# Kernel optimization log

Hardware: AMD Instinct MI355X
Metric: run time of the kernel (lower is better)

Reference implementation:

```python
import jax, jax.numpy as jnp
import numpy as np
import math

B, T, D, H = 1, 2048, 1024, 16
DH = D // H  # 64


def relative_shift(x):
    # x: [B, H, T, S] -> Transformer-XL relative shift via zero-pad + reshape
    b, h, t, s = x.shape
    zero_pad = jnp.zeros((b, h, t, 1), dtype=x.dtype)
    x_padded = jnp.concatenate([zero_pad, x], axis=-1)       # [B,H,T,S+1]
    x_padded = x_padded.reshape(b, h, s + 1, t)              # [B,H,S+1,T]
    return x_padded[:, :, 1:].reshape(b, h, t, s)            # [B,H,T,S]


def setup_inputs() -> dict:
    key = jax.random.key(0)
    ks = jax.random.split(key, 9)
    std = 0.02
    return {
        "x": jax.random.normal(ks[0], (B, T, D), dtype=jnp.float32),
        "r_emb": jax.random.normal(ks[1], (T, D), dtype=jnp.float32),
        "Wq": jax.random.normal(ks[2], (D, D), dtype=jnp.float32) * std,
        "Wk": jax.random.normal(ks[3], (D, D), dtype=jnp.float32) * std,
        "Wv": jax.random.normal(ks[4], (D, D), dtype=jnp.float32) * std,
        "Wr": jax.random.normal(ks[5], (D, D), dtype=jnp.float32) * std,
        "Wo": jax.random.normal(ks[6], (D, D), dtype=jnp.float32) * std,
        "u": jax.random.normal(ks[7], (H, DH), dtype=jnp.float32) * std,
        "v_bias": jax.random.normal(ks[8], (H, DH), dtype=jnp.float32) * std,
    }


def reference(x, r_emb, Wq, Wk, Wv, Wr, Wo, u, v_bias):
    # mem=None path (the only shape-consistent path in the source), so S == T.
    b, t, d = x.shape
    s = t
    q = (x @ Wq).reshape(b, t, H, DH).transpose(0, 2, 1, 3)   # [B,H,T,DH]
    k = (x @ Wk).reshape(b, s, H, DH).transpose(0, 2, 1, 3)   # [B,H,S,DH]
    v = (x @ Wv).reshape(b, s, H, DH).transpose(0, 2, 1, 3)   # [B,H,S,DH]
    r = (r_emb @ Wr).reshape(r_emb.shape[0], H, DH)[-s:]       # [S,H,DH]

    AC = jnp.einsum('bhid,bhjd->bhij', q + u[None, :, None, :], k)
    BD = jnp.einsum('bhid,jhd->bhij', q + v_bias[None, :, None, :], r)
    BD = relative_shift(BD)

    attn = (AC + BD) / math.sqrt(DH)                           # [B,H,T,S]
    mask = jnp.tril(jnp.ones((t, s), dtype=bool))              # causal (S==T)
    attn = jnp.where(mask[None, None], attn, -jnp.inf)
    attn = jax.nn.softmax(attn, axis=-1)
    # dropout is identity in eval mode
    out = jnp.einsum('bhij,bhjd->bhid', attn, v)               # [B,H,T,DH]
    out = out.transpose(0, 2, 1, 3).reshape(b, t, d)           # [B,T,D]
    return out @ Wo
```

## Files before the change

kernel.cpp:

```cpp
#include <hip/hip_runtime.h>

typedef __bf16 bf16_t;
typedef __bf16 bf16x4v __attribute__((ext_vector_type(4)));
typedef __bf16 bf16x8 __attribute__((ext_vector_type(8)));
typedef float f32x4 __attribute__((ext_vector_type(4)));

constexpr int TT = 2048;
constexpr int DDIM = 1024;

constexpr size_t SZ_TD  = (size_t)2048 * 1024;
constexpr size_t OFF_QU = 0;
constexpr size_t OFF_QV = 1 * SZ_TD;
constexpr size_t OFF_KK = 2 * SZ_TD;
constexpr size_t OFF_RR = 3 * SZ_TD;
constexpr size_t OFF_VT = 4 * SZ_TD;
constexpr size_t OFF_AO = 5 * SZ_TD;
constexpr size_t OFF_XB = 6 * SZ_TD;
constexpr size_t OFF_RB = 7 * SZ_TD;
constexpr size_t OFF_WT = 8 * SZ_TD;
constexpr size_t SZ_W   = (size_t)1024 * 1024;
constexpr size_t OFF_P2 = OFF_WT + SZ_W;

__device__ __forceinline__ f32x4 fzero4() {
  f32x4 z; z[0] = 0.f; z[1] = 0.f; z[2] = 0.f; z[3] = 0.f; return z;
}

__device__ __forceinline__ void gload16(const bf16_t* g, bf16_t* l) {
  __builtin_amdgcn_global_load_lds((const __attribute__((address_space(1))) void*)g,
                                   (__attribute__((address_space(3))) void*)l, 16, 0, 0);
}

__global__ __launch_bounds__(256) void convert_kernel(const float* __restrict__ x,
                                                      const float* __restrict__ r,
                                                      bf16_t* __restrict__ ws) {
  const int i = blockIdx.x * 256 + threadIdx.x;
  float4 a = ((const float4*)x)[i];
  float4 b = ((const float4*)r)[i];
  bf16x4v av, bv;
  av[0] = (bf16_t)a.x; av[1] = (bf16_t)a.y; av[2] = (bf16_t)a.z; av[3] = (bf16_t)a.w;
  bv[0] = (bf16_t)b.x; bv[1] = (bf16_t)b.y; bv[2] = (bf16_t)b.z; bv[3] = (bf16_t)b.w;
  ((bf16x4v*)(ws + OFF_XB))[i] = av;
  ((bf16x4v*)(ws + OFF_RB))[i] = bv;
}

__global__ __launch_bounds__(256) void transpose_w_kernel(const float* __restrict__ Wq,
                                                          const float* __restrict__ Wk,
                                                          const float* __restrict__ Wv,
                                                          const float* __restrict__ Wr,
                                                          const float* __restrict__ Wo,
                                                          bf16_t* __restrict__ ws) {
  const int k0 = blockIdx.x * 64, n0 = blockIdx.y * 64, wsel = blockIdx.z;
  const float* W = (wsel == 0) ? Wq : (wsel == 1) ? Wk : (wsel == 2) ? Wv : (wsel == 3) ? Wr : Wo;
  bf16_t* Wt = ws + OFF_WT + (size_t)wsel * SZ_W;
  __shared__ float tile[64][65];
  const int tid = threadIdx.x;
#pragma unroll
  for (int it = 0; it < 4; ++it) {
    int g = tid + it * 256; int rr = g >> 4; int c4 = (g & 15) * 4;
    float4 v = *(const float4*)&W[(size_t)(k0 + rr) * DDIM + n0 + c4];
    tile[rr][c4] = v.x; tile[rr][c4 + 1] = v.y; tile[rr][c4 + 2] = v.z; tile[rr][c4 + 3] = v.w;
  }
  __syncthreads();
#pragma unroll
  for (int it = 0; it < 4; ++it) {
    int g = tid + it * 256; int nr = g >> 4; int c4 = (g & 15) * 4;
    bf16x4v o;
    o[0] = (bf16_t)tile[c4 + 0][nr]; o[1] = (bf16_t)tile[c4 + 1][nr];
    o[2] = (bf16_t)tile[c4 + 2][nr]; o[3] = (bf16_t)tile[c4 + 3][nr];
    *(bf16x4v*)&Wt[(size_t)(n0 + nr) * DDIM + k0 + c4] = o;
  }
}

__device__ __forceinline__ void gemm128_core(const bf16_t* __restrict__ A,
                                             const bf16_t* __restrict__ Bt,
                                             int i0, int n0, int kbeg, int kend,
                                             f32x4 acc[4][4],
                                             bf16_t* As, bf16_t* Bs) {
  const int tid = threadIdx.x, lane = tid & 63, wv = tid >> 6;
  const int wr = (wv >> 1) * 64, wc = (wv & 1) * 64;
  const int sr = tid >> 2, scc = (tid & 3) * 8;
  const int l15 = lane & 15, lg8 = (lane >> 4) * 8;
  for (int k0 = kbeg; k0 < kend; k0 += 32) {
    __syncthreads();
    gload16(&A[(size_t)(i0 + sr) * DDIM + k0 + scc],       &As[sr * 32 + scc]);
    gload16(&A[(size_t)(i0 + 64 + sr) * DDIM + k0 + scc],  &As[(64 + sr) * 32 + scc]);
    gload16(&Bt[(size_t)(n0 + sr) * DDIM + k0 + scc],      &Bs[sr * 32 + scc]);
    gload16(&Bt[(size_t)(n0 + 64 + sr) * DDIM + k0 + scc], &Bs[(64 + sr) * 32 + scc]);
    __syncthreads();
    bf16x8 af[4], bfv[4];
#pragma unroll
    for (int m = 0; m < 4; ++m) af[m] = *(const bf16x8*)&As[(wr + m * 16 + l15) * 32 + lg8];
#pragma unroll
    for (int n = 0; n < 4; ++n) bfv[n] = *(const bf16x8*)&Bs[(wc + n * 16 + l15) * 32 + lg8];
#pragma unroll
    for (int m = 0; m < 4; ++m)
#pragma unroll
      for (int n = 0; n < 4; ++n)
        acc[m][n] = __builtin_amdgcn_mfma_f32_16x16x32_bf16(af[m], bfv[n], acc[m][n], 0, 0, 0);
  }
}

__global__ __launch_bounds__(256) void proj_kernel(const bf16_t* wsc, bf16_t* wsd,
                                                   const float* __restrict__ u,
                                                   const float* __restrict__ vb) {
  const int z = blockIdx.z;
  const int i0 = blockIdx.x * 128, n0 = blockIdx.y * 64;
  const bf16_t* A = wsc + ((z == 3) ? OFF_RB : OFF_XB);
  const bf16_t* Bt = wsc + OFF_WT + (size_t)z * SZ_W;
  __shared__ bf16_t As[128 * 32];
  __shared__ bf16_t Bs[64 * 32];
  const int tid = threadIdx.x, lane = tid & 63, wv = tid >> 6;
  const int wr = (wv >> 1) * 64, wc = (wv & 1) * 32;
  const int sr = tid >> 2, scc = (tid & 3) * 8;
  const int l15 = lane & 15, lg8 = (lane >> 4) * 8, lr4 = (lane >> 4) * 4;
  f32x4 acc[4][2];
#pragma unroll
  for (int m = 0; m < 4; ++m)
#pragma unroll
    for (int n = 0; n < 2; ++n) acc[m][n] = fzero4();

  for (int k0 = 0; k0 < DDIM; k0 += 32) {
    __syncthreads();
    gload16(&A[(size_t)(i0 + sr) * DDIM + k0 + scc],      &As[sr * 32 + scc]);
    gload16(&A[(size_t)(i0 + 64 + sr) * DDIM + k0 + scc], &As[(64 + sr) * 32 + scc]);
    gload16(&Bt[(size_t)(n0 + sr) * DDIM + k0 + scc],     &Bs[sr * 32 + scc]);
    __syncthreads();
    bf16x8 af[4], bfv[2];
#pragma unroll
    for (int m = 0; m < 4; ++m) af[m] = *(const bf16x8*)&As[(wr + m * 16 + l15) * 32 + lg8];
#pragma unroll
    for (int n = 0; n < 2; ++n) bfv[n] = *(const bf16x8*)&Bs[(wc + n * 16 + l15) * 32 + lg8];
#pragma unroll
    for (int m = 0; m < 4; ++m)
#pragma unroll
      for (int n = 0; n < 2; ++n)
        acc[m][n] = __builtin_amdgcn_mfma_f32_16x16x32_bf16(af[m], bfv[n], acc[m][n], 0, 0, 0);
  }

#pragma unroll
  for (int mm = 0; mm < 4; ++mm)
#pragma unroll
    for (int nn = 0; nn < 2; ++nn)
#pragma unroll
      for (int rg = 0; rg < 4; ++rg) {
        const int row = i0 + wr + mm * 16 + lr4 + rg;
        const int col = n0 + wc + nn * 16 + l15;
        const float val = acc[mm][nn][rg];
        const int hh = col >> 6, dh = col & 63;
        if (z == 0) {
          wsd[OFF_QU + ((size_t)hh * TT + row) * 64 + dh] = (bf16_t)(val + u[col]);
          wsd[OFF_QV + ((size_t)hh * TT + row) * 64 + dh] = (bf16_t)(val + vb[col]);
        } else if (z == 1) {
          wsd[OFF_KK + ((size_t)hh * TT + row) * 64 + dh] = (bf16_t)val;
        } else if (z == 2) {
          wsd[OFF_VT + ((size_t)hh * 64 + dh) * TT + row] = (bf16_t)val;
        } else {
          wsd[OFF_RR + ((size_t)hh * TT + (TT - 1 - row)) * 64 + dh] = (bf16_t)val;
        }
      }
}

#define LOADK(DST, JJ)                                                                     \
  _Pragma("unroll") for (int nt_ = 0; nt_ < 4; ++nt_)                                      \
  _Pragma("unroll") for (int ks_ = 0; ks_ < 2; ++ks_)                                      \
    DST[nt_][ks_] = *(const bf16x8*)&Kp[(size_t)((JJ) + nt_ * 16 + l15) * 64 + ks_ * 32 + lg8];

#define ATTN_BODY(KC, KN, J0, JN)                                                          \
  {                                                                                        \
    bf16x8 rf[5][2];                                                                       \
    const int c0 = iw0 - (J0) - 63;                                                        \
    _Pragma("unroll") for (int bt = 0; bt < 5; ++bt) {                                     \
      int c = c0 + bt * 16 + l15;                                                          \
      c = (c < 0) ? 0 : ((c > TT - 1) ? TT - 1 : c);                                       \
      _Pragma("unroll") for (int ks = 0; ks < 2; ++ks)                                     \
        rf[bt][ks] = *(const bf16x8*)&Rp[(size_t)c * 64 + ks * 32 + lg8];                  \
    }                                                                                      \
    bf16x8 vf[4][2];                                                                       \
    _Pragma("unroll") for (int d = 0; d < 4; ++d)                                          \
      _Pragma("unroll") for (int ks = 0; ks < 2; ++ks)                                     \
        vf[d][ks] = *(const bf16x8*)&Vp[(size_t)(d * 16 + l15) * TT + (J0) + ks * 32 + lg8];\
    LOADK(KN, JN)                                                                          \
    f32x4 ac[4];                                                                           \
    _Pragma("unroll") for (int nt = 0; nt < 4; ++nt) ac[nt] = fzero4();                    \
    _Pragma("unroll") for (int nt = 0; nt < 4; ++nt)                                       \
      _Pragma("unroll") for (int ks = 0; ks < 2; ++ks)                                     \
        ac[nt] = __builtin_amdgcn_mfma_f32_16x16x32_bf16(KC[nt][ks], qu[ks], ac[nt], 0, 0, 0); \
    f32x4 bd[5];                                                                           \
    _Pragma("unroll") for (int bt = 0; bt < 5; ++bt) bd[bt] = fzero4();                    \
    _Pragma("unroll") for (int bt = 0; bt < 5; ++bt)                                       \
      _Pragma("unroll") for (int ks = 0; ks < 2; ++ks)                                     \
        bd[bt] = __builtin_amdgcn_mfma_f32_16x16x32_bf16(rf[bt][ks], qv[ks], bd[bt], 0, 0, 0); \
    _Pragma("unroll") for (int bt = 0; bt < 5; ++bt)                                       \
      _Pragma("unroll") for (int rg = 0; rg < 4; ++rg)                                     \
        PB[(bt * 16 + lg * 4 + rg) * 17 + l15] = bd[bt][rg];                               \
    float sc[4][4];                                                                        \
    float smax = -3e38f;                                                                   \
    _Pragma("unroll") for (int nt = 0; nt < 4; ++nt)                                       \
      _Pragma("unroll") for (int rg = 0; rg < 4; ++rg) {                                   \
        const int jj = nt * 16 + lg * 4 + rg;                                              \
        float v = (ac[nt][rg] + PB[(l15 + 63 - jj) * 17 + l15]) * 0.125f;                  \
        v = ((J0) + jj > iw0 + l15) ? -1e30f : v;                                          \
        smax = fmaxf(smax, v);                                                             \
        sc[nt][rg] = v;                                                                    \
      }                                                                                    \
    smax = fmaxf(smax, __shfl_xor(smax, 16));                                              \
    smax = fmaxf(smax, __shfl_xor(smax, 32));                                              \
    const float newm = fmaxf(mrun, smax);                                                  \
    const float fac = __expf(mrun - newm);                                                 \
    mrun = newm;                                                                           \
    float pv[4][4];                                                                        \
    float rsum = 0.f;                                                                      \
    _Pragma("unroll") for (int nt = 0; nt < 4; ++nt)                                       \
      _Pragma("unroll") for (int rg = 0; rg < 4; ++rg) {                                   \
        pv[nt][rg] = __expf(sc[nt][rg] - newm);                                            \
        rsum += pv[nt][rg];                                                                \
      }                                                                                    \
    rsum += __shfl_xor(rsum, 16);                                                          \
    rsum += __shfl_xor(rsum, 32);                                                          \
    lrun = lrun * fac + rsum;                                                              \
    float fo[4];                                                                           \
    _Pragma("unroll") for (int rg = 0; rg < 4; ++rg) fo[rg] = __shfl(fac, lg * 4 + rg);    \
    _Pragma("unroll") for (int d = 0; d < 4; ++d)                                          \
      _Pragma("unroll") for (int rg = 0; rg < 4; ++rg) o[d][rg] *= fo[rg];                 \
    _Pragma("unroll") for (int nt = 0; nt < 4; ++nt) {                                     \
      bf16x4v pk;                                                                          \
      pk[0] = (bf16_t)pv[nt][0]; pk[1] = (bf16_t)pv[nt][1];                                \
      pk[2] = (bf16_t)pv[nt][2]; pk[3] = (bf16_t)pv[nt][3];                                \
      *(bf16x4v*)&PL[l15 * 72 + nt * 16 + lg * 4] = pk;                                    \
    }                                                                                      \
    bf16x8 pf[2];                                                                          \
    _Pragma("unroll") for (int ks = 0; ks < 2; ++ks)                                       \
      pf[ks] = *(const bf16x8*)&PL[l15 * 72 + ks * 32 + lg8];                              \
    _Pragma("unroll") for (int d = 0; d < 4; ++d)                                          \
      _Pragma("unroll") for (int ks = 0; ks < 2; ++ks)                                     \
        o[d] = __builtin_amdgcn_mfma_f32_16x16x32_bf16(pf[ks], vf[d][ks], o[d], 0, 0, 0);  \
  }

__global__ __launch_bounds__(64) void attn_kernel(const bf16_t* wsc, bf16_t* wsd) {
  const int h = blockIdx.x;
  const int chunk = blockIdx.z;
  const int q16 = 127 - blockIdx.y;
  const int iw0 = q16 * 16;
  const int lane = threadIdx.x & 63;
  const int l15 = lane & 15;
  const int lg = lane >> 4;
  const int lg8 = lg * 8;

  const int NT = (q16 >> 2) + 1;
  const int base = NT / 3, rem = NT % 3;
  const int tbeg = chunk * base + (chunk < rem ? chunk : rem);
  const int tend = tbeg + base + (chunk < rem ? 1 : 0);

  bf16_t* Po = wsd + ((chunk == 0) ? OFF_XB : (chunk == 1) ? OFF_RB : OFF_P2)
             + (size_t)h * TT * 64;
  float2* ml = (float2*)(wsd + OFF_WT) + (size_t)(chunk * 16 + h) * TT;

  if (tbeg >= tend) {
#pragma unroll
    for (int d = 0; d < 4; ++d)
#pragma unroll
      for (int rg = 0; rg < 4; ++rg)
        Po[(size_t)(iw0 + lg * 4 + rg) * 64 + d * 16 + l15] = (bf16_t)0.f;
    if (lg == 0) ml[iw0 + l15] = make_float2(-3e38f, 0.f);
    return;
  }

  const bf16_t* QUp = wsc + OFF_QU + (size_t)h * TT * 64;
  const bf16_t* QVp = wsc + OFF_QV + (size_t)h * TT * 64;
  const bf16_t* Kp  = wsc + OFF_KK + (size_t)h * TT * 64;
  const bf16_t* Rp  = wsc + OFF_RR + (size_t)h * TT * 64;
  const bf16_t* Vp  = wsc + OFF_VT + (size_t)h * 64 * TT;

  __shared__ float PB[80 * 17];
  __shared__ bf16_t PL[16 * 72];

  bf16x8 qu[2], qv[2];
#pragma unroll
  for (int ks = 0; ks < 2; ++ks) {
    qu[ks] = *(const bf16x8*)&QUp[(size_t)(iw0 + l15) * 64 + ks * 32 + lg8];
    qv[ks] = *(const bf16x8*)&QVp[(size_t)(iw0 + l15) * 64 + ks * 32 + lg8];
  }

  f32x4 o[4];
#pragma unroll
  for (int d = 0; d < 4; ++d) o[d] = fzero4();
  float mrun = -3e38f, lrun = 0.f;

  bf16x8 kA[4][2], kB[4][2];
  LOADK(kA, tbeg * 64)

  int t = tbeg;
  while (true) {
    int j0 = t * 64;
    int tn = (t + 1 < tend) ? t + 1 : t;
    ATTN_BODY(kA, kB, j0, tn * 64)
    if (++t >= tend) break;
    j0 = t * 64;
    tn = (t + 1 < tend) ? t + 1 : t;
    ATTN_BODY(kB, kA, j0, tn * 64)
    if (++t >= tend) break;
  }

#pragma unroll
  for (int d = 0; d < 4; ++d)
#pragma unroll
    for (int rg = 0; rg < 4; ++rg)
      Po[(size_t)(iw0 + lg * 4 + rg) * 64 + d * 16 + l15] = (bf16_t)o[d][rg];
  if (lg == 0) ml[iw0 + l15] = make_float2(mrun, lrun);
}

__global__ __launch_bounds__(256) void combine_kernel(const bf16_t* wsc, bf16_t* wsd) {
  const int gid = blockIdx.x * 256 + threadIdx.x;
  const int row = gid >> 3;
  const int colg = (gid & 7) * 8;
  const float2* mlp = (const float2*)(wsc + OFF_WT);
  const float2 ml0 = mlp[row];
  const float2 ml1 = mlp[16 * TT + row];
  const float2 ml2 = mlp[32 * TT + row];
  const float M = fmaxf(fmaxf(ml0.x, ml1.x), ml2.x);
  const float e0 = __expf(ml0.x - M), e1 = __expf(ml1.x - M), e2 = __expf(ml2.x - M);
  const float inv = 1.f / (ml0.y * e0 + ml1.y * e1 + ml2.y * e2);
  bf16x8 o0 = *(const bf16x8*)&wsc[OFF_XB + (size_t)row * 64 + colg];
  bf16x8 o1 = *(const bf16x8*)&wsc[OFF_RB + (size_t)row * 64 + colg];
  bf16x8 o2 = *(const bf16x8*)&wsc[OFF_P2 + (size_t)row * 64 + colg];
  const int hh = row >> 11, tt2 = row & 2047;
  bf16x8 r;
#pragma unroll
  for (int i = 0; i < 8; ++i)
    r[i] = (bf16_t)(((float)o0[i] * e0 + (float)o1[i] * e1 + (float)o2[i] * e2) * inv);
  *(bf16x8*)&wsd[OFF_AO + (size_t)tt2 * DDIM + hh * 64 + colg] = r;
}

__global__ __launch_bounds__(256) void outproj_kernel(const bf16_t* wsc, float* __restrict__ outp) {
  const int i0 = blockIdx.x * 128, n0 = blockIdx.y * 128, kz = blockIdx.z;
  const bf16_t* A = wsc + OFF_AO;
  const bf16_t* Bt = wsc + OFF_WT + 4 * SZ_W;
  __shared__ bf16_t As[128 * 32];
  __shared__ bf16_t Bs[128 * 32];
  const int lane = threadIdx.x & 63, wv = threadIdx.x >> 6;
  const int wr = (wv >> 1) * 64, wc = (wv & 1) * 64;
  const int l15 = lane & 15, lr4 = (lane >> 4) * 4;
  f32x4 acc[4][4];
#pragma unroll
  for (int m = 0; m < 4; ++m)
#pragma unroll
    for (int n = 0; n < 4; ++n) acc[m][n] = fzero4();

  gemm128_core(A, Bt, i0, n0, kz * 256, kz * 256 + 256, acc, As, Bs);

#pragma unroll
  for (int mm = 0; mm < 4; ++mm)
#pragma unroll
    for (int nn = 0; nn < 4; ++nn)
#pragma unroll
      for (int rg = 0; rg < 4; ++rg) {
        const int row = i0 + wr + mm * 16 + lr4 + rg;
        const int col = n0 + wc + nn * 16 + l15;
        atomicAdd(&outp[(size_t)row * DDIM + col], acc[mm][nn][rg]);
      }
}

extern "C" void kernel_launch(void* const* d_in, const int* in_sizes, int n_in,
                              void* d_out, int out_size, void* d_ws, size_t ws_size,
                              hipStream_t stream) {
  (void)in_sizes; (void)n_in; (void)out_size; (void)ws_size;
  const float* x    = (const float*)d_in[0];
  const float* remb = (const float*)d_in[1];
  const float* Wq   = (const float*)d_in[2];
  const float* Wk   = (const float*)d_in[3];
  const float* Wv   = (const float*)d_in[4];
  const float* Wr   = (const float*)d_in[5];
  const float* Wo   = (const float*)d_in[6];
  const float* u    = (const float*)d_in[7];
  const float* vb   = (const float*)d_in[8];
  bf16_t* ws = (bf16_t*)d_ws;
  float* outp = (float*)d_out;

  hipMemsetAsync(outp, 0, (size_t)TT * DDIM * sizeof(float), stream);
  convert_kernel<<<dim3(2048), 256, 0, stream>>>(x, remb, ws);
  transpose_w_kernel<<<dim3(16, 16, 5), 256, 0, stream>>>(Wq, Wk, Wv, Wr, Wo, ws);
  proj_kernel<<<dim3(16, 16, 4), 256, 0, stream>>>(ws, ws, u, vb);
  attn_kernel<<<dim3(16, 128, 3), 64, 0, stream>>>(ws, ws);
  combine_kernel<<<dim3(1024), 256, 0, stream>>>(ws, ws);
  outproj_kernel<<<dim3(16, 8, 4), 256, 0, stream>>>(ws, outp);
}
```

Baseline: 276.5 us.

## Process two 16-row query tiles per wave sharing K/R/V fragment loads

Each attention wave now handles 32 query rows as two 16-row tiles that share the same K, V and most of the R fragments per 64-key block. The split-KV factor drops from three chunks to two, and the combine kernel merges two partials instead of three. The K double-buffer prefetch is removed in favour of a simple loop. The aim is to cut redundant global loads and combine traffic, at the cost of fewer blocks (less parallelism) and higher register pressure.

```diff
diff --git a/kernel.cpp b/kernel.cpp
--- a/kernel.cpp
+++ b/kernel.cpp
@@ -19,7 +19,6 @@
 constexpr size_t OFF_RB = 7 * SZ_TD;
 constexpr size_t OFF_WT = 8 * SZ_TD;
 constexpr size_t SZ_W   = (size_t)1024 * 1024;
-constexpr size_t OFF_P2 = OFF_WT + SZ_W;
 
 __device__ __forceinline__ f32x4 fzero4() {
   f32x4 z; z[0] = 0.f; z[1] = 0.f; z[2] = 0.f; z[3] = 0.f; return z;
@@ -160,54 +159,23 @@
       }
 }
 
-#define LOADK(DST, JJ)                                                                     \
-  _Pragma("unroll") for (int nt_ = 0; nt_ < 4; ++nt_)                                      \
-  _Pragma("unroll") for (int ks_ = 0; ks_ < 2; ++ks_)                                      \
-    DST[nt_][ks_] = *(const bf16x8*)&Kp[(size_t)((JJ) + nt_ * 16 + l15) * 64 + ks_ * 32 + lg8];
-
-#define ATTN_BODY(KC, KN, J0, JN)                                                          \
+#define SOFTPV(AC, PBX, PLX, QBASE, OO, MRUN, LRUN)                                        \
   {                                                                                        \
-    bf16x8 rf[5][2];                                                                       \
-    const int c0 = iw0 - (J0) - 63;                                                        \
-    _Pragma("unroll") for (int bt = 0; bt < 5; ++bt) {                                     \
-      int c = c0 + bt * 16 + l15;                                                          \
-      c = (c < 0) ? 0 : ((c > TT - 1) ? TT - 1 : c);                                       \
-      _Pragma("unroll") for (int ks = 0; ks < 2; ++ks)                                     \
-        rf[bt][ks] = *(const bf16x8*)&Rp[(size_t)c * 64 + ks * 32 + lg8];                  \
-    }                                                                                      \
-    bf16x8 vf[4][2];                                                                       \
-    _Pragma("unroll") for (int d = 0; d < 4; ++d)                                          \
-      _Pragma("unroll") for (int ks = 0; ks < 2; ++ks)                                     \
-        vf[d][ks] = *(const bf16x8*)&Vp[(size_t)(d * 16 + l15) * TT + (J0) + ks * 32 + lg8];\
-    LOADK(KN, JN)                                                                          \
-    f32x4 ac[4];                                                                           \
-    _Pragma("unroll") for (int nt = 0; nt < 4; ++nt) ac[nt] = fzero4();                    \
-    _Pragma("unroll") for (int nt = 0; nt < 4; ++nt)                                       \
-      _Pragma("unroll") for (int ks = 0; ks < 2; ++ks)                                     \
-        ac[nt] = __builtin_amdgcn_mfma_f32_16x16x32_bf16(KC[nt][ks], qu[ks], ac[nt], 0, 0, 0); \
-    f32x4 bd[5];                                                                           \
-    _Pragma("unroll") for (int bt = 0; bt < 5; ++bt) bd[bt] = fzero4();                    \
-    _Pragma("unroll") for (int bt = 0; bt < 5; ++bt)                                       \
-      _Pragma("unroll") for (int ks = 0; ks < 2; ++ks)                                     \
-        bd[bt] = __builtin_amdgcn_mfma_f32_16x16x32_bf16(rf[bt][ks], qv[ks], bd[bt], 0, 0, 0); \
-    _Pragma("unroll") for (int bt = 0; bt < 5; ++bt)                                       \
-      _Pragma("unroll") for (int rg = 0; rg < 4; ++rg)                                     \
-        PB[(bt * 16 + lg * 4 + rg) * 17 + l15] = bd[bt][rg];                               \
     float sc[4][4];                                                                        \
     float smax = -3e38f;                                                                   \
     _Pragma("unroll") for (int nt = 0; nt < 4; ++nt)                                       \
       _Pragma("unroll") for (int rg = 0; rg < 4; ++rg) {                                   \
         const int jj = nt * 16 + lg * 4 + rg;                                              \
-        float v = (ac[nt][rg] + PB[(l15 + 63 - jj) * 17 + l15]) * 0.125f;                  \
-        v = ((J0) + jj > iw0 + l15) ? -1e30f : v;                                          \
+        float v = (AC[nt][rg] + PBX[(l15 + 63 - jj) * 18 + l15]) * 0.125f;                 \
+        v = (j0 + jj > (QBASE) + l15) ? -1e30f : v;                                        \
         smax = fmaxf(smax, v);                                                             \
         sc[nt][rg] = v;                                                                    \
       }                                                                                    \
     smax = fmaxf(smax, __shfl_xor(smax, 16));                                              \
     smax = fmaxf(smax, __shfl_xor(smax, 32));                                              \
-    const float newm = fmaxf(mrun, smax);                                                  \
-    const float fac = __expf(mrun - newm);                                                 \
-    mrun = newm;                                                                           \
+    const float newm = fmaxf(MRUN, smax);                                                  \
+    const float fac = __expf(MRUN - newm);                                                 \
+    MRUN = newm;                                                                           \
     float pv[4][4];                                                                        \
     float rsum = 0.f;                                                                      \
     _Pragma("unroll") for (int nt = 0; nt < 4; ++nt)                                       \
@@ -217,51 +185,52 @@
       }                                                                                    \
     rsum += __shfl_xor(rsum, 16);                                                          \
     rsum += __shfl_xor(rsum, 32);                                                          \
-    lrun = lrun * fac + rsum;                                                              \
+    LRUN = LRUN * fac + rsum;                                                              \
     float fo[4];                                                                           \
     _Pragma("unroll") for (int rg = 0; rg < 4; ++rg) fo[rg] = __shfl(fac, lg * 4 + rg);    \
     _Pragma("unroll") for (int d = 0; d < 4; ++d)                                          \
-      _Pragma("unroll") for (int rg = 0; rg < 4; ++rg) o[d][rg] *= fo[rg];                 \
+      _Pragma("unroll") for (int rg = 0; rg < 4; ++rg) OO[d][rg] *= fo[rg];                \
     _Pragma("unroll") for (int nt = 0; nt < 4; ++nt) {                                     \
       bf16x4v pk;                                                                          \
       pk[0] = (bf16_t)pv[nt][0]; pk[1] = (bf16_t)pv[nt][1];                                \
       pk[2] = (bf16_t)pv[nt][2]; pk[3] = (bf16_t)pv[nt][3];                                \
-      *(bf16x4v*)&PL[l15 * 72 + nt * 16 + lg * 4] = pk;                                    \
+      *(bf16x4v*)&PLX[l15 * 72 + nt * 16 + lg * 4] = pk;                                   \
     }                                                                                      \
     bf16x8 pf[2];                                                                          \
     _Pragma("unroll") for (int ks = 0; ks < 2; ++ks)                                       \
-      pf[ks] = *(const bf16x8*)&PL[l15 * 72 + ks * 32 + lg8];                              \
+      pf[ks] = *(const bf16x8*)&PLX[l15 * 72 + ks * 32 + lg8];                             \
     _Pragma("unroll") for (int d = 0; d < 4; ++d)                                          \
       _Pragma("unroll") for (int ks = 0; ks < 2; ++ks)                                     \
-        o[d] = __builtin_amdgcn_mfma_f32_16x16x32_bf16(pf[ks], vf[d][ks], o[d], 0, 0, 0);  \
+        OO[d] = __builtin_amdgcn_mfma_f32_16x16x32_bf16(pf[ks], vf[d][ks], OO[d], 0, 0, 0);\
   }
 
 __global__ __launch_bounds__(64) void attn_kernel(const bf16_t* wsc, bf16_t* wsd) {
   const int h = blockIdx.x;
   const int chunk = blockIdx.z;
-  const int q16 = 127 - blockIdx.y;
-  const int iw0 = q16 * 16;
+  const int q32 = 63 - blockIdx.y;
+  const int i0 = q32 * 32;
   const int lane = threadIdx.x & 63;
   const int l15 = lane & 15;
   const int lg = lane >> 4;
   const int lg8 = lg * 8;
 
-  const int NT = (q16 >> 2) + 1;
-  const int base = NT / 3, rem = NT % 3;
-  const int tbeg = chunk * base + (chunk < rem ? chunk : rem);
-  const int tend = tbeg + base + (chunk < rem ? 1 : 0);
-
-  bf16_t* Po = wsd + ((chunk == 0) ? OFF_XB : (chunk == 1) ? OFF_RB : OFF_P2)
-             + (size_t)h * TT * 64;
+  const int NT = (i0 >> 6) + 1;
+  const int H = (NT + 1) >> 1;
+  const int tbeg = chunk ? H : 0;
+  const int tend = chunk ? NT : H;
+
+  bf16_t* Po = wsd + ((chunk == 0) ? OFF_XB : OFF_RB) + (size_t)h * TT * 64;
   float2* ml = (float2*)(wsd + OFF_WT) + (size_t)(chunk * 16 + h) * TT;
 
   if (tbeg >= tend) {
 #pragma unroll
-    for (int d = 0; d < 4; ++d)
-#pragma unroll
-      for (int rg = 0; rg < 4; ++rg)
-        Po[(size_t)(iw0 + lg * 4 + rg) * 64 + d * 16 + l15] = (bf16_t)0.f;
-    if (lg == 0) ml[iw0 + l15] = make_float2(-3e38f, 0.f);
+    for (int m = 0; m < 2; ++m)
+#pragma unroll
+      for (int d = 0; d < 4; ++d)
+#pragma unroll
+        for (int rg = 0; rg < 4; ++rg)
+          Po[(size_t)(i0 + m * 16 + lg * 4 + rg) * 64 + d * 16 + l15] = (bf16_t)0.f;
+    if (lg == 0) { ml[i0 + l15] = make_float2(-3e38f, 0.f); ml[i0 + 16 + l15] = make_float2(-3e38f, 0.f); }
     return;
   }
 
@@ -271,42 +240,89 @@
   const bf16_t* Rp  = wsc + OFF_RR + (size_t)h * TT * 64;
   const bf16_t* Vp  = wsc + OFF_VT + (size_t)h * 64 * TT;
 
-  __shared__ float PB[80 * 17];
-  __shared__ bf16_t PL[16 * 72];
-
-  bf16x8 qu[2], qv[2];
+  __shared__ float PB1[80 * 18];
+  __shared__ float PB2[80 * 18];
+  __shared__ bf16_t PL1[16 * 72];
+  __shared__ bf16_t PL2[16 * 72];
+
+  bf16x8 qu1[2], qv1[2], qu2[2], qv2[2];
 #pragma unroll
   for (int ks = 0; ks < 2; ++ks) {
-    qu[ks] = *(const bf16x8*)&QUp[(size_t)(iw0 + l15) * 64 + ks * 32 + lg8];
-    qv[ks] = *(const bf16x8*)&QVp[(size_t)(iw0 + l15) * 64 + ks * 32 + lg8];
-  }
-
-  f32x4 o[4];
-#pragma unroll
-  for (int d = 0; d < 4; ++d) o[d] = fzero4();
-  float mrun = -3e38f, lrun = 0.f;
-
-  bf16x8 kA[4][2], kB[4][2];
-  LOADK(kA, tbeg * 64)
-
-  int t = tbeg;
-  while (true) {
-    int j0 = t * 64;
-    int tn = (t + 1 < tend) ? t + 1 : t;
-    ATTN_BODY(kA, kB, j0, tn * 64)
-    if (++t >= tend) break;
-    j0 = t * 64;
-    tn = (t + 1 < tend) ? t + 1 : t;
-    ATTN_BODY(kB, kA, j0, tn * 64)
-    if (++t >= tend) break;
+    qu1[ks] = *(const bf16x8*)&QUp[(size_t)(i0 + l15) * 64 + ks * 32 + lg8];
+    qv1[ks] = *(const bf16x8*)&QVp[(size_t)(i0 + l15) * 64 + ks * 32 + lg8];
+    qu2[ks] = *(const bf16x8*)&QUp[(size_t)(i0 + 16 + l15) * 64 + ks * 32 + lg8];
+    qv2[ks] = *(const bf16x8*)&QVp[(size_t)(i0 + 16 + l15) * 64 + ks * 32 + lg8];
+  }
+
+  f32x4 o1[4], o2[4];
+#pragma unroll
+  for (int d = 0; d < 4; ++d) { o1[d] = fzero4(); o2[d] = fzero4(); }
+  float m1 = -3e38f, l1 = 0.f, m2 = -3e38f, l2 = 0.f;
+
+  for (int t = tbeg; t < tend; ++t) {
+    const int j0 = t * 64;
+    bf16x8 kf[4][2], rf[6][2], vf[4][2];
+#pragma unroll
+    for (int nt = 0; nt < 4; ++nt)
+#pragma unroll
+      for (int ks = 0; ks < 2; ++ks)
+        kf[nt][ks] = *(const bf16x8*)&Kp[(size_t)(j0 + nt * 16 + l15) * 64 + ks * 32 + lg8];
+    const int c0 = i0 - j0 - 63;
+#pragma unroll
+    for (int bt = 0; bt < 6; ++bt) {
+      int c = c0 + bt * 16 + l15;
+      c = (c < 0) ? 0 : ((c > TT - 1) ? TT - 1 : c);
+#pragma unroll
+      for (int ks = 0; ks < 2; ++ks)
+        rf[bt][ks] = *(const bf16x8*)&Rp[(size_t)c * 64 + ks * 32 + lg8];
+    }
+#pragma unroll
+    for (int d = 0; d < 4; ++d)
+#pragma unroll
+      for (int ks = 0; ks < 2; ++ks)
+        vf[d][ks] = *(const bf16x8*)&Vp[(size_t)(d * 16 + l15) * TT + j0 + ks * 32 + lg8];
+
+    f32x4 ac1[4], ac2[4];
+#pragma unroll
+    for (int nt = 0; nt < 4; ++nt) { ac1[nt] = fzero4(); ac2[nt] = fzero4(); }
+#pragma unroll
+    for (int nt = 0; nt < 4; ++nt)
+#pragma unroll
+      for (int ks = 0; ks < 2; ++ks) {
+        ac1[nt] = __builtin_amdgcn_mfma_f32_16x16x32_bf16(kf[nt][ks], qu1[ks], ac1[nt], 0, 0, 0);
+        ac2[nt] = __builtin_amdgcn_mfma_f32_16x16x32_bf16(kf[nt][ks], qu2[ks], ac2[nt], 0, 0, 0);
+      }
+
+    f32x4 bd1[5], bd2[5];
+#pragma unroll
+    for (int bt = 0; bt < 5; ++bt) { bd1[bt] = fzero4(); bd2[bt] = fzero4(); }
+#pragma unroll
+    for (int bt = 0; bt < 5; ++bt)
+#pragma unroll
+      for (int ks = 0; ks < 2; ++ks) {
+        bd1[bt] = __builtin_amdgcn_mfma_f32_16x16x32_bf16(rf[bt][ks], qv1[ks], bd1[bt], 0, 0, 0);
+        bd2[bt] = __builtin_amdgcn_mfma_f32_16x16x32_bf16(rf[bt + 1][ks], qv2[ks], bd2[bt], 0, 0, 0);
+      }
+#pragma unroll
+    for (int bt = 0; bt < 5; ++bt)
+#pragma unroll
+      for (int rg = 0; rg < 4; ++rg) {
+        PB1[(bt * 16 + lg * 4 + rg) * 18 + l15] = bd1[bt][rg];
+        PB2[(bt * 16 + lg * 4 + rg) * 18 + l15] = bd2[bt][rg];
+      }
+
+    SOFTPV(ac1, PB1, PL1, i0, o1, m1, l1)
+    SOFTPV(ac2, PB2, PL2, i0 + 16, o2, m2, l2)
   }
 
 #pragma unroll
   for (int d = 0; d < 4; ++d)
 #pragma unroll
-    for (int rg = 0; rg < 4; ++rg)
-      Po[(size_t)(iw0 + lg * 4 + rg) * 64 + d * 16 + l15] = (bf16_t)o[d][rg];
-  if (lg == 0) ml[iw0 + l15] = make_float2(mrun, lrun);
+    for (int rg = 0; rg < 4; ++rg) {
+      Po[(size_t)(i0 + lg * 4 + rg) * 64 + d * 16 + l15] = (bf16_t)o1[d][rg];
+      Po[(size_t)(i0 + 16 + lg * 4 + rg) * 64 + d * 16 + l15] = (bf16_t)o2[d][rg];
+    }
+  if (lg == 0) { ml[i0 + l15] = make_float2(m1, l1); ml[i0 + 16 + l15] = make_float2(m2, l2); }
 }
 
 __global__ __launch_bounds__(256) void combine_kernel(const bf16_t* wsc, bf16_t* wsd) {
@@ -316,18 +332,16 @@
   const float2* mlp = (const float2*)(wsc + OFF_WT);
   const float2 ml0 = mlp[row];
   const float2 ml1 = mlp[16 * TT + row];
-  const float2 ml2 = mlp[32 * TT + row];
-  const float M = fmaxf(fmaxf(ml0.x, ml1.x), ml2.x);
-  const float e0 = __expf(ml0.x - M), e1 = __expf(ml1.x - M), e2 = __expf(ml2.x - M);
-  const float inv = 1.f / (ml0.y * e0 + ml1.y * e1 + ml2.y * e2);
+  const float M = fmaxf(ml0.x, ml1.x);
+  const float e0 = __expf(ml0.x - M), e1 = __expf(ml1.x - M);
+  const float inv = 1.f / (ml0.y * e0 + ml1.y * e1);
   bf16x8 o0 = *(const bf16x8*)&wsc[OFF_XB + (size_t)row * 64 + colg];
   bf16x8 o1 = *(const bf16x8*)&wsc[OFF_RB + (size_t)row * 64 + colg];
-  bf16x8 o2 = *(const bf16x8*)&wsc[OFF_P2 + (size_t)row * 64 + colg];
   const int hh = row >> 11, tt2 = row & 2047;
   bf16x8 r;
 #pragma unroll
   for (int i = 0; i < 8; ++i)
-    r[i] = (bf16_t)(((float)o0[i] * e0 + (float)o1[i] * e1 + (float)o2[i] * e2) * inv);
+    r[i] = (bf16_t)(((float)o0[i] * e0 + (float)o1[i] * e1) * inv);
   *(bf16x8*)&wsd[OFF_AO + (size_t)tt2 * DDIM + hh * 64 + colg] = r;
 }
 
@@ -380,7 +394,7 @@
   convert_kernel<<<dim3(2048), 256, 0, stream>>>(x, remb, ws);
   transpose_w_kernel<<<dim3(16, 16, 5), 256, 0, stream>>>(Wq, Wk, Wv, Wr, Wo, ws);
   proj_kernel<<<dim3(16, 16, 4), 256, 0, stream>>>(ws, ws, u, vb);
-  attn_kernel<<<dim3(16, 128, 3), 64, 0, stream>>>(ws, ws);
+  attn_kernel<<<dim3(16, 64, 2), 64, 0, stream>>>(ws, ws);
   combine_kernel<<<dim3(1024), 256, 0, stream>>>(ws, ws);
   outproj_kernel<<<dim3(16, 8, 4), 256, 0, stream>>>(ws, outp);
 }
```

After: 229.4 us. -17.0%, faster.
